# Kernel tuning notes

Hardware: AMD Instinct MI355X
Metric: run time of the kernel (lower is better)

## Reference

```python
import jax, jax.numpy as jnp
import numpy as np

N_NODES = 100000
N_EDGES = 1600000
IN_DIM = 128
HID_DIM = 128
OUT_DIM = 64
BN_EPS = 1e-5


def setup_inputs() -> dict:
    key = jax.random.key(0)
    ks = jax.random.split(key, 8)
    x = jax.random.normal(ks[0], (N_NODES, IN_DIM), dtype=jnp.float32)
    edge_index = jax.random.randint(ks[1], (2, N_EDGES), 0, N_NODES, dtype=jnp.int64)
    s1 = 1.0 / np.sqrt(IN_DIM)
    s2 = 1.0 / np.sqrt(HID_DIM)
    return {
        "x": x,
        "edge_index": edge_index,
        "W1l": jax.random.normal(ks[2], (HID_DIM, IN_DIM), dtype=jnp.float32) * s1,
        "b1l": jnp.zeros((HID_DIM,), dtype=jnp.float32),
        "W1r": jax.random.normal(ks[3], (HID_DIM, IN_DIM), dtype=jnp.float32) * s1,
        "bn_gamma": jnp.ones((HID_DIM,), dtype=jnp.float32),
        "bn_beta": jnp.zeros((HID_DIM,), dtype=jnp.float32),
        "bn_mean": jnp.zeros((HID_DIM,), dtype=jnp.float32),
        "bn_var": jnp.ones((HID_DIM,), dtype=jnp.float32),
        "W2l": jax.random.normal(ks[4], (OUT_DIM, HID_DIM), dtype=jnp.float32) * s2,
        "b2l": jnp.zeros((OUT_DIM,), dtype=jnp.float32),
        "W2r": jax.random.normal(ks[5], (OUT_DIM, HID_DIM), dtype=jnp.float32) * s2,
    }


def _sage_conv(x, src, dst, Wl, bl, Wr, num_nodes):
    # message = x[src], mean-aggregated at dst; out = lin_l(agg) + lin_r(x)
    msgs = x[src]  # [E, D] gather (memory bound)
    agg = jax.ops.segment_sum(msgs, dst, num_segments=num_nodes)
    deg = jax.ops.segment_sum(jnp.ones((src.shape[0],), dtype=x.dtype), dst,
                              num_segments=num_nodes)
    agg = agg / jnp.maximum(deg, 1.0)[:, None]
    return agg @ Wl.T + bl + x @ Wr.T


def reference(x, edge_index, W1l, b1l, W1r, bn_gamma, bn_beta, bn_mean, bn_var,
              W2l, b2l, W2r):
    src, dst = edge_index[0], edge_index[1]
    n = x.shape[0]
    h = _sage_conv(x, src, dst, W1l, b1l, W1r, n)
    # BatchNorm1d (inference: running stats), then ReLU; dropout is identity in eval
    h = (h - bn_mean) * (bn_gamma * jax.lax.rsqrt(bn_var + BN_EPS)) + bn_beta
    h = jax.nn.relu(h)
    return _sage_conv(h, src, dst, W2l, b2l, W2r, n)
```

## Files before the change

### kernel.cpp

```cpp
#include <hip/hip_runtime.h>
#include <hip/hip_fp16.h>

#define N_NODES 100000
#define N_EDGES 1600000
#define TILE 2048
#define NBUK 64
#define BSH 11
#define NBUK_USED ((N_NODES + (1 << BSH) - 1) >> BSH)
#define CAP 36864
#define SMASK 0x1FFFF
#define PRE_BLOCKS 12500
#define BINA_BLOCKS ((N_EDGES + TILE - 1) / TILE)

typedef _Float16 f16x8 __attribute__((ext_vector_type(8)));
typedef float    f32x4 __attribute__((ext_vector_type(4)));

__global__ __launch_bounds__(256) void k_preA(
    const float* __restrict__ x, __half* __restrict__ x_h,
    const float* __restrict__ W1l, const float* __restrict__ W1r,
    const float* __restrict__ W2l, const float* __restrict__ W2r,
    __half* __restrict__ W1lf, __half* __restrict__ W1rf,
    __half* __restrict__ W2f,
    const int* __restrict__ ei, int* __restrict__ bcur,
    int2* __restrict__ ebuf)
{
    __shared__ int2 scratch[TILE];
    __shared__ int hist[NBUK];
    __shared__ int tstart[NBUK];
    __shared__ int gbase[NBUK];
    int t = threadIdx.x;

    if (blockIdx.x < PRE_BLOCKS) {
        int i = blockIdx.x * 256 + t;
        if (i < N_NODES * 32) {
            float4 v = ((const float4*)x)[i];
            __half2 a = __floats2half2_rn(v.x, v.y);
            __half2 b = __floats2half2_rn(v.z, v.w);
            uint2 u = make_uint2(*(unsigned*)&a, *(unsigned*)&b);
            ((uint2*)x_h)[i] = u;
        }
        if (i < 49152) {
            int tt = i & 16383;
            int j    = tt & 7;
            int lane = (tt >> 3) & 63;
            int ks   = (tt >> 9) & 3;
            int ct   = tt >> 11;
            int m = lane & 15, q = lane >> 4;
            int row = ct * 16 + m;
            int col = ks * 32 + q * 8 + j;
            if (i < 16384) {
                W1lf[tt] = __float2half(W1l[row * 128 + col]);
            } else if (i < 32768) {
                W1rf[tt] = __float2half(W1r[row * 128 + col]);
            } else {
                float v = (ct < 4) ? W2l[row * 128 + col]
                                   : W2r[(row - 64) * 128 + col];
                W2f[tt] = __float2half(v);
            }
        }
        return;
    }

    int e0 = (blockIdx.x - PRE_BLOCKS) * TILE;
    int tile_n = min(TILE, N_EDGES - e0);
    if (t < NBUK) hist[t] = 0;
    __syncthreads();
    int srcs[8], dsts[8], rank[8], bks[8];
    #pragma unroll
    for (int i = 0; i < 8; ++i) {
        int e = e0 + i * 256 + t;
        bks[i] = -1;
        if (e < N_EDGES) {
            srcs[i] = ei[e];
            dsts[i] = ei[N_EDGES + e];
            bks[i]  = (dsts[i] >> BSH) & (NBUK - 1);
            rank[i] = atomicAdd(&hist[bks[i]], 1);
        }
    }
    __syncthreads();
    if (t == 0) {
        int s = 0;
        #pragma unroll
        for (int b = 0; b < NBUK; ++b) { tstart[b] = s; s += hist[b]; }
    }
    __syncthreads();
    if (t < NBUK && hist[t] > 0)
        gbase[t] = t * CAP + atomicAdd(&bcur[t], hist[t]);
    __syncthreads();
    #pragma unroll
    for (int i = 0; i < 8; ++i)
        if (bks[i] >= 0) {
            int sl = tstart[bks[i]] + rank[i];
            scratch[min(sl, TILE - 1)] = make_int2(srcs[i], dsts[i]);
        }
    __syncthreads();
    for (int p = t; p < tile_n; p += 256) {
        int2 sd = scratch[p];
        int b = (sd.y >> BSH) & (NBUK - 1);
        int o = gbase[b] + (p - tstart[b]);
        ebuf[min(max(o, 0), NBUK * CAP - 1)] = sd;
    }
}

__global__ __launch_bounds__(1024) void k_fillC2(
    const int2* __restrict__ ebuf, const int* __restrict__ bcur,
    int* __restrict__ row_ptr, int* __restrict__ csr_src)
{
    __shared__ int hist[1 << BSH];
    __shared__ int psum[1024];
    __shared__ int cur[1 << BSH];
    __shared__ int bb_l[NBUK_USED + 1];
    int t = threadIdx.x;
    int b = blockIdx.x;
    int base = b << BSH;
    hist[t] = 0;
    hist[t + 1024] = 0;
    if (t < 64) {
        int c = (t < NBUK_USED) ? bcur[t] : 0;
        c = min(max(c, 0), CAP);
        int s = c;
        #pragma unroll
        for (int off = 1; off < 64; off <<= 1) {
            int v = __shfl_up(s, off);
            if (t >= off) s += v;
        }
        if (t < NBUK_USED) bb_l[t] = s - c;
        if (t == NBUK_USED - 1) bb_l[NBUK_USED] = s;
    }
    __syncthreads();
    int bb  = bb_l[b];
    int cnt = min(bb_l[b + 1] - bb, CAP);
    const int2* eb = ebuf + (size_t)b * CAP;
    for (int p = t; p < cnt; p += 1024)
        atomicAdd(&hist[(eb[p].y - base) & ((1 << BSH) - 1)], 1);
    __syncthreads();
    int h0 = hist[2 * t], h1 = hist[2 * t + 1];
    psum[t] = h0 + h1;
    __syncthreads();
    #pragma unroll
    for (int off = 1; off < 1024; off <<= 1) {
        int v = (t >= off) ? psum[t - off] : 0;
        __syncthreads();
        psum[t] += v;
        __syncthreads();
    }
    int e0 = bb + psum[t] - (h0 + h1);
    int e1 = e0 + h0;
    int n0g = base + 2 * t, n1g = n0g + 1;
    if (n0g <= N_NODES) row_ptr[n0g] = e0;
    if (n1g <= N_NODES) row_ptr[n1g] = e1;
    cur[2 * t]     = e0;
    cur[2 * t + 1] = e1;
    __syncthreads();
    for (int p = t; p < cnt; p += 1024) {
        int2 sd = eb[p];
        int pos = atomicAdd(&cur[(sd.y - base) & ((1 << BSH) - 1)], 1);
        csr_src[min(max(pos, 0), N_EDGES - 1)] = sd.x;
    }
}

__device__ __forceinline__ void acc_row8h(
    const __half* __restrict__ x_h, int s, int col,
    __half2& a0, __half2& a1)
{
    uint2 u = ((const uint2*)(x_h + (size_t)(s & SMASK) * 128))[col];
    a0 = __hadd2(a0, *(__half2*)&u.x);
    a1 = __hadd2(a1, *(__half2*)&u.y);
}

__global__ __launch_bounds__(256) void k_agg1(
    const int* __restrict__ row_ptr, const int* __restrict__ csr_src,
    const __half* __restrict__ x_h, __half* __restrict__ agg_h)
{
    int tid  = threadIdx.x;
    int lane = tid & 63;
    int half = lane >> 5;
    int col  = lane & 31;
    int n    = blockIdx.x * 4 + (tid >> 6);
    int e1 = min(row_ptr[n + 1], N_EDGES);
    int e0 = min(max(row_ptr[n], 0), e1);
    __half2 a0 = __floats2half2_rn(0.f, 0.f);
    __half2 a1 = a0;
    for (int eb = e0; eb < e1; eb += 64) {
        int cnt = min(e1 - eb, 64);
        int sv = csr_src[min(eb + lane, N_EDGES - 1)];
        int j = 0;
        for (; j + 16 <= cnt; j += 16) {
            int sr[8];
            #pragma unroll
            for (int u = 0; u < 8; ++u) {
                int sa = __builtin_amdgcn_readlane(sv, j + 2 * u);
                int sb = __builtin_amdgcn_readlane(sv, j + 2 * u + 1);
                sr[u] = half ? sb : sa;
            }
            #pragma unroll
            for (int u = 0; u < 8; ++u)
                acc_row8h(x_h, sr[u], col, a0, a1);
        }
        for (; j + 8 <= cnt; j += 8) {
            int sr[4];
            #pragma unroll
            for (int u = 0; u < 4; ++u) {
                int sa = __builtin_amdgcn_readlane(sv, j + 2 * u);
                int sb = __builtin_amdgcn_readlane(sv, j + 2 * u + 1);
                sr[u] = half ? sb : sa;
            }
            #pragma unroll
            for (int u = 0; u < 4; ++u)
                acc_row8h(x_h, sr[u], col, a0, a1);
        }
        for (; j + 2 <= cnt; j += 2) {
            int sa = __builtin_amdgcn_readlane(sv, j);
            int sb = __builtin_amdgcn_readlane(sv, j + 1);
            int s  = half ? sb : sa;
            acc_row8h(x_h, s, col, a0, a1);
        }
        if (j < cnt) {
            int sa = __builtin_amdgcn_readlane(sv, j);
            if (half == 0) acc_row8h(x_h, sa, col, a0, a1);
        }
    }
    unsigned v0 = *(unsigned*)&a0, v1 = *(unsigned*)&a1;
    unsigned o0 = (unsigned)__shfl_xor((int)v0, 32);
    unsigned o1 = (unsigned)__shfl_xor((int)v1, 32);
    a0 = __hadd2(a0, *(__half2*)&o0);
    a1 = __hadd2(a1, *(__half2*)&o1);
    if (half == 0) {
        uint2 u = make_uint2(*(unsigned*)&a0, *(unsigned*)&a1);
        ((uint2*)agg_h)[n * 32 + col] = u;
    }
}

__global__ __launch_bounds__(256) void k_g12(
    const __half* __restrict__ agg_h, const int* __restrict__ row_ptr,
    const __half* __restrict__ x_h,
    const __half* __restrict__ W1lf, const float* __restrict__ b1l,
    const __half* __restrict__ W1rf,
    const float* __restrict__ gamma, const float* __restrict__ beta,
    const float* __restrict__ mean, const float* __restrict__ var,
    const __half* __restrict__ W2f, const float* __restrict__ b2l,
    __half* __restrict__ p2, float* __restrict__ out)
{
    __shared__ __half Ah[16][64][8];
    int tid  = threadIdx.x;
    int lane = tid & 63;
    int w    = tid >> 6;
    int m    = lane & 15;
    int q    = lane >> 4;
    int n0   = blockIdx.x * 64;

    int arow = n0 + w * 16 + m;
    bool aok = arow < N_NODES;
    const __half* pa = agg_h + (size_t)(aok ? arow : 0) * 128 + q * 8;
    const __half* px = x_h   + (size_t)(aok ? arow : 0) * 128 + q * 8;
    f16x8 aL[4], aR[4];
    #pragma unroll
    for (int ks = 0; ks < 4; ++ks) {
        f16x8 va = {}, vx = {};
        if (aok) {
            va = *(const f16x8*)(pa + ks * 32);
            vx = *(const f16x8*)(px + ks * 32);
        }
        aL[ks] = va;
        aR[ks] = vx;
    }
    const __half* bl0 = W1lf + (lane << 3);
    const __half* br0 = W1rf + (lane << 3);
    f32x4 accL[8], accR[8];
    #pragma unroll
    for (int c = 0; c < 8; ++c) {
        accL[c] = (f32x4){0.f, 0.f, 0.f, 0.f};
        accR[c] = (f32x4){0.f, 0.f, 0.f, 0.f};
    }
    #pragma unroll
    for (int ks = 0; ks < 4; ++ks) {
        #pragma unroll
        for (int ct = 0; ct < 8; ++ct) {
            f16x8 bL = *(const f16x8*)(bl0 + ((ct * 4 + ks) << 9));
            f16x8 bR = *(const f16x8*)(br0 + ((ct * 4 + ks) << 9));
            accL[ct] = __builtin_amdgcn_mfma_f32_16x16x32_f16(aL[ks], bL, accL[ct], 0, 0, 0);
            accR[ct] = __builtin_amdgcn_mfma_f32_16x16x32_f16(aR[ks], bR, accR[ct], 0, 0, 0);
        }
    }
    float invd[4];
    #pragma unroll
    for (int r = 0; r < 4; ++r) {
        int n = n0 + w * 16 + q * 4 + r;
        int d = (n < N_NODES) ? (row_ptr[n + 1] - row_ptr[n]) : 1;
        invd[r] = 1.0f / fmaxf((float)d, 1.0f);
    }
    #pragma unroll
    for (int ct = 0; ct < 8; ++ct) {
        int col = ct * 16 + m;
        float s = gamma[col] * rsqrtf(var[col] + 1e-5f);
        float t = beta[col] + (b1l[col] - mean[col]) * s;
        #pragma unroll
        for (int r = 0; r < 4; ++r) {
            float v = accL[ct][r] * invd[r] + accR[ct][r];
            v = fmaxf(v * s + t, 0.f);
            Ah[col >> 3][w * 16 + q * 4 + r][col & 7] = __float2half(v);
        }
    }
    __syncthreads();
    const __half* b0 = W2f + (lane << 3);
    f32x4 acc2[8];
    #pragma unroll
    for (int c = 0; c < 8; ++c) acc2[c] = (f32x4){0.f, 0.f, 0.f, 0.f};
    #pragma unroll
    for (int ks = 0; ks < 4; ++ks) {
        f16x8 a = *(const f16x8*)&Ah[ks * 4 + q][w * 16 + m][0];
        #pragma unroll
        for (int ct = 0; ct < 8; ++ct) {
            f16x8 b = *(const f16x8*)(b0 + ((ct * 4 + ks) << 9));
            acc2[ct] = __builtin_amdgcn_mfma_f32_16x16x32_f16(a, b, acc2[ct], 0, 0, 0);
        }
    }
    #pragma unroll
    for (int r = 0; r < 4; ++r) {
        int ng = n0 + w * 16 + q * 4 + r;
        if (ng < N_NODES) {
            #pragma unroll
            for (int ct = 0; ct < 4; ++ct)
                p2[(size_t)ng * 64 + ct * 16 + m] = __float2half(acc2[ct][r]);
            #pragma unroll
            for (int ct = 4; ct < 8; ++ct) {
                int c = (ct - 4) * 16 + m;
                out[(size_t)ng * 64 + c] = acc2[ct][r] + b2l[c];
            }
        }
    }
}

__device__ __forceinline__ void acc_row_p2h(
    const __half* __restrict__ p2, int s, int lane,
    __half2& a0, __half2& a1)
{
    uint2 u = ((const uint2*)(p2 + (size_t)(s & SMASK) * 64))[lane];
    a0 = __hadd2(a0, *(__half2*)&u.x);
    a1 = __hadd2(a1, *(__half2*)&u.y);
}

__global__ __launch_bounds__(256) void k_agg2(
    const int* __restrict__ row_ptr, const int* __restrict__ csr_src,
    const __half* __restrict__ p2, float* __restrict__ out)
{
    int tid  = threadIdx.x;
    int n    = blockIdx.x * 16 + (tid >> 4);
    int lane = tid & 15;
    int e1 = min(row_ptr[n + 1], N_EDGES);
    int e0 = min(max(row_ptr[n], 0), e1);
    __half2 a0 = __floats2half2_rn(0.f, 0.f);
    __half2 a1 = a0;
    int e = e0;
    for (; e + 8 <= e1; e += 8) {
        int s[8];
        #pragma unroll
        for (int u = 0; u < 8; ++u) s[u] = csr_src[e + u];
        #pragma unroll
        for (int u = 0; u < 8; ++u) acc_row_p2h(p2, s[u], lane, a0, a1);
    }
    for (; e + 4 <= e1; e += 4) {
        int s[4];
        #pragma unroll
        for (int u = 0; u < 4; ++u) s[u] = csr_src[e + u];
        #pragma unroll
        for (int u = 0; u < 4; ++u) acc_row_p2h(p2, s[u], lane, a0, a1);
    }
    for (; e < e1; ++e) acc_row_p2h(p2, csr_src[e], lane, a0, a1);
    float inv = 1.0f / fmaxf((float)(e1 - e0), 1.0f);
    float2 f0 = __half22float2(a0);
    float2 f1 = __half22float2(a1);
    float4* o = (float4*)out + n * 16 + lane;
    float4 cur = *o;
    cur.x += f0.x * inv; cur.y += f0.y * inv;
    cur.z += f1.x * inv; cur.w += f1.y * inv;
    *o = cur;
}

extern "C" void kernel_launch(void* const* d_in, const int* in_sizes, int n_in,
                              void* d_out, int out_size, void* d_ws, size_t ws_size,
                              hipStream_t stream)
{
    const float* x     = (const float*)d_in[0];
    const int*   ei    = (const int*)d_in[1];
    const float* W1l   = (const float*)d_in[2];
    const float* b1l   = (const float*)d_in[3];
    const float* W1r   = (const float*)d_in[4];
    const float* gamma = (const float*)d_in[5];
    const float* beta  = (const float*)d_in[6];
    const float* mean  = (const float*)d_in[7];
    const float* var   = (const float*)d_in[8];
    const float* W2l   = (const float*)d_in[9];
    const float* b2l   = (const float*)d_in[10];
    const float* W2r   = (const float*)d_in[11];
    float* out = (float*)d_out;

    char* ws = (char*)d_ws;
    __half* agg_h   = (__half*)(ws);
    __half* p2      = (__half*)(ws + 25600000);
    __half* x_h     = (__half*)(ws + 51200000);
    int*    csr_src = (int*)(ws + 76800000);
    int*    row_ptr = (int*)(ws + 83200000);
    __half* W1lf    = (__half*)(ws + 83600016);
    __half* W1rf    = (__half*)(ws + 83632784);
    __half* W2f     = (__half*)(ws + 83665552);
    int2*   ebuf    = (int2*)(ws + 83698320);
    int*    bcur    = (int*)(ws + 102572688);

    hipMemsetAsync(bcur, 0, NBUK * sizeof(int), stream);
    k_preA<<<PRE_BLOCKS + BINA_BLOCKS, 256, 0, stream>>>(
        x, x_h, W1l, W1r, W2l, W2r, W1lf, W1rf, W2f, ei, bcur, ebuf);
    k_fillC2<<<NBUK_USED, 1024, 0, stream>>>(ebuf, bcur, row_ptr, csr_src);
    k_agg1<<<N_NODES / 4, 256, 0, stream>>>(row_ptr, csr_src, x_h, agg_h);
    k_g12<<<(N_NODES + 63) / 64, 256, 0, stream>>>(agg_h, row_ptr, x_h,
                                                   W1lf, b1l, W1rf,
                                                   gamma, beta, mean, var,
                                                   W2f, b2l, p2, out);
    k_agg2<<<N_NODES / 16, 256, 0, stream>>>(row_ptr, csr_src, p2, out);
}
```

Before: 308.2 us.

## Balance k_agg2 edge work across block via shared-memory atomic accumulation

The layer-2 aggregation kernel now treats the block's 16 nodes as one contiguous edge range. Each 16-lane group strides over edges, finds the owning node by binary search over cached row pointers, and accumulates into a shared-memory fp32 tile with atomics. This removes load imbalance between nodes of different degree and switches accumulation from fp16 to fp32. The cost is LDS atomic traffic and search overhead for every edge.

After: 805.2 us. 161% more time.

```diff
diff --git a/kernel.cpp b/kernel.cpp
--- a/kernel.cpp
+++ b/kernel.cpp
@@ -331,50 +331,82 @@
     }
 }
 
-__device__ __forceinline__ void acc_row_p2h(
-    const __half* __restrict__ p2, int s, int lane,
-    __half2& a0, __half2& a1)
-{
-    uint2 u = ((const uint2*)(p2 + (size_t)(s & SMASK) * 64))[lane];
-    a0 = __hadd2(a0, *(__half2*)&u.x);
-    a1 = __hadd2(a1, *(__half2*)&u.y);
-}
-
 __global__ __launch_bounds__(256) void k_agg2(
     const int* __restrict__ row_ptr, const int* __restrict__ csr_src,
     const __half* __restrict__ p2, float* __restrict__ out)
 {
+    __shared__ float acc[16][68];
+    __shared__ int rp[17];
     int tid  = threadIdx.x;
-    int n    = blockIdx.x * 16 + (tid >> 4);
+    int n0   = blockIdx.x * 16;
+    int grp  = tid >> 4;
     int lane = tid & 15;
-    int e1 = min(row_ptr[n + 1], N_EDGES);
-    int e0 = min(max(row_ptr[n], 0), e1);
-    __half2 a0 = __floats2half2_rn(0.f, 0.f);
-    __half2 a1 = a0;
-    int e = e0;
-    for (; e + 8 <= e1; e += 8) {
-        int s[8];
-        #pragma unroll
-        for (int u = 0; u < 8; ++u) s[u] = csr_src[e + u];
-        #pragma unroll
-        for (int u = 0; u < 8; ++u) acc_row_p2h(p2, s[u], lane, a0, a1);
-    }
-    for (; e + 4 <= e1; e += 4) {
-        int s[4];
-        #pragma unroll
-        for (int u = 0; u < 4; ++u) s[u] = csr_src[e + u];
-        #pragma unroll
-        for (int u = 0; u < 4; ++u) acc_row_p2h(p2, s[u], lane, a0, a1);
-    }
-    for (; e < e1; ++e) acc_row_p2h(p2, csr_src[e], lane, a0, a1);
-    float inv = 1.0f / fmaxf((float)(e1 - e0), 1.0f);
-    float2 f0 = __half22float2(a0);
-    float2 f1 = __half22float2(a1);
-    float4* o = (float4*)out + n * 16 + lane;
-    float4 cur = *o;
-    cur.x += f0.x * inv; cur.y += f0.y * inv;
-    cur.z += f1.x * inv; cur.w += f1.y * inv;
-    *o = cur;
+
+    if (tid < 17) {
+        int v = row_ptr[n0 + tid];
+        rp[tid] = min(max(v, 0), N_EDGES);
+    }
+    for (int i = tid; i < 16 * 68; i += 256)
+        ((float*)acc)[i] = 0.f;
+    __syncthreads();
+
+    int e0 = rp[0], e1 = rp[16];
+    int e = e0 + grp;
+    for (; e + 48 < e1; e += 64) {
+        int es[4], ss[4], rr[4];
+        #pragma unroll
+        for (int u = 0; u < 4; ++u) es[u] = e + u * 16;
+        #pragma unroll
+        for (int u = 0; u < 4; ++u) ss[u] = csr_src[es[u]];
+        #pragma unroll
+        for (int u = 0; u < 4; ++u) {
+            int r = 0;
+            #pragma unroll
+            for (int step = 8; step >= 1; step >>= 1)
+                if (r + step < 16 && rp[r + step] <= es[u]) r += step;
+            rr[u] = r;
+        }
+        #pragma unroll
+        for (int u = 0; u < 4; ++u) {
+            uint2 v = ((const uint2*)(p2 + (size_t)(ss[u] & SMASK) * 64))[lane];
+            float2 f0 = __half22float2(*(__half2*)&v.x);
+            float2 f1 = __half22float2(*(__half2*)&v.y);
+            float* row = &acc[rr[u]][lane * 4];
+            atomicAdd(row + 0, f0.x);
+            atomicAdd(row + 1, f0.y);
+            atomicAdd(row + 2, f1.x);
+            atomicAdd(row + 3, f1.y);
+        }
+    }
+    for (; e < e1; e += 16) {
+        int s = csr_src[e];
+        int r = 0;
+        #pragma unroll
+        for (int step = 8; step >= 1; step >>= 1)
+            if (r + step < 16 && rp[r + step] <= e) r += step;
+        uint2 v = ((const uint2*)(p2 + (size_t)(s & SMASK) * 64))[lane];
+        float2 f0 = __half22float2(*(__half2*)&v.x);
+        float2 f1 = __half22float2(*(__half2*)&v.y);
+        float* row = &acc[r][lane * 4];
+        atomicAdd(row + 0, f0.x);
+        atomicAdd(row + 1, f0.y);
+        atomicAdd(row + 2, f1.x);
+        atomicAdd(row + 3, f1.y);
+    }
+    __syncthreads();
+
+    {
+        int rrow = tid >> 4;
+        int cc   = tid & 15;
+        int deg  = rp[rrow + 1] - rp[rrow];
+        float inv = 1.0f / fmaxf((float)deg, 1.0f);
+        float4 v = *(float4*)&acc[rrow][cc * 4];
+        float4* o = (float4*)(out + (size_t)(n0 + rrow) * 64) + cc;
+        float4 cur = *o;
+        cur.x += v.x * inv; cur.y += v.y * inv;
+        cur.z += v.z * inv; cur.w += v.w * inv;
+        *o = cur;
+    }
 }
 
 extern "C" void kernel_launch(void* const* d_in, const int* in_sizes, int n_in,
```
